# Performance work log

Hardware: AMD Instinct MI355X
Metric: run time of the kernel (lower is better)

## Reference

```python
import jax, jax.numpy as jnp
import numpy as np

D_STATE = 8
DT_RANK = 8  # ceil(128/16)


def _grouped_1x1(x, w):
    # x: (B,H,W,Cin), w: (g, Cout//g, Cin//g)
    B, H, W, _ = x.shape
    g, o, i = w.shape
    xg = x.reshape(B, H, W, g, i)
    return jnp.einsum('bhwgi,goi->bhwgo', xg, w).reshape(B, H, W, g * o)


def setup_inputs() -> dict:
    key = jax.random.key(0)
    ks = jax.random.split(key, 16)
    B, H, W, C = 8, 64, 64, 128
    g = 4
    D = 128  # expand_dim = d_inner
    N = D_STATE
    R = DT_RANK
    inp = {}
    inp['x'] = jax.random.normal(ks[0], (B, H, W, C), dtype=jnp.float32)
    inp['w1'] = jax.random.normal(ks[1], (g, D // g, C // g), dtype=jnp.float32) * 0.1
    inp['dw'] = jax.random.normal(ks[2], (3, 3, 1, D), dtype=jnp.float32) * 0.1  # HWIO depthwise
    inp['in_proj_w'] = jax.random.normal(ks[3], (2 * D, D), dtype=jnp.float32) * 0.05
    inp['conv1d_w'] = jax.random.normal(ks[4], (D, 3), dtype=jnp.float32) * 0.1
    inp['conv1d_b'] = jax.random.normal(ks[5], (D,), dtype=jnp.float32) * 0.05
    inp['x_proj_w'] = jax.random.normal(ks[6], (R + 2 * N, D), dtype=jnp.float32) * 0.05
    inp['dt_proj_w'] = jax.random.normal(ks[7], (D, R), dtype=jnp.float32) * 0.05
    inp['dt_proj_b'] = jax.random.normal(ks[8], (D,), dtype=jnp.float32) * 0.05
    inp['A_log'] = jnp.log(jnp.tile(jnp.arange(1, N + 1, dtype=jnp.float32)[None, :], (D, 1)))
    inp['D_param'] = jnp.ones((D,), dtype=jnp.float32)
    inp['out_proj_w'] = jax.random.normal(ks[9], (D, D), dtype=jnp.float32) * 0.05
    inp['gamma'] = jnp.ones((D,), dtype=jnp.float32)
    inp['beta'] = jnp.zeros((D,), dtype=jnp.float32)
    inp['w2'] = jax.random.normal(ks[10], (g, D // g, C // g), dtype=jnp.float32) * 0.1
    inp['wout'] = jax.random.normal(ks[11], (g, C // g, D // g), dtype=jnp.float32) * 0.1
    return inp


def _mamba(x_seq, in_proj_w, conv1d_w, conv1d_b, x_proj_w, dt_proj_w, dt_proj_b, A_log, D_param, out_proj_w):
    # x_seq: (B, L, D)
    B, L, D = x_seq.shape
    N, R = D_STATE, DT_RANK
    xz = jnp.einsum('bld,ed->ble', x_seq, in_proj_w)  # (B,L,2D)
    u, z = xz[..., :D], xz[..., D:]
    # causal depthwise conv1d, kernel=3, left pad 2 (torch: padding=2, slice [:L])
    up = jnp.pad(u, ((0, 0), (2, 0), (0, 0)))
    u = (up[:, 0:L] * conv1d_w[:, 0] + up[:, 1:L + 1] * conv1d_w[:, 1]
         + up[:, 2:L + 2] * conv1d_w[:, 2] + conv1d_b)
    u = jax.nn.silu(u)
    x_dbl = jnp.einsum('bld,ed->ble', u, x_proj_w)  # (B,L,R+2N)
    dt = x_dbl[..., :R]
    Bm = x_dbl[..., R:R + N]
    Cm = x_dbl[..., R + N:]
    delta = jax.nn.softplus(jnp.einsum('blr,dr->bld', dt, dt_proj_w) + dt_proj_b)  # (B,L,D)
    A = -jnp.exp(A_log)  # (D,N)

    def step(h, inp):
        d_t, u_t, b_t, c_t = inp  # (B,D),(B,D),(B,N),(B,N)
        dA = jnp.exp(d_t[..., None] * A)            # (B,D,N)
        h = dA * h + (d_t * u_t)[..., None] * b_t[:, None, :]
        y_t = jnp.einsum('bdn,bn->bd', h, c_t)
        return h, y_t

    h0 = jnp.zeros((B, D, N), dtype=x_seq.dtype)
    xs = (jnp.swapaxes(delta, 0, 1), jnp.swapaxes(u, 0, 1),
          jnp.swapaxes(Bm, 0, 1), jnp.swapaxes(Cm, 0, 1))
    _, ys = jax.lax.scan(step, h0, xs)              # ys: (L,B,D)
    y = jnp.swapaxes(ys, 0, 1) + u * D_param
    y = y * jax.nn.silu(z)
    return jnp.einsum('bld,ed->ble', y, out_proj_w)


def reference(x, w1, dw, in_proj_w, conv1d_w, conv1d_b, x_proj_w, dt_proj_w, dt_proj_b,
              A_log, D_param, out_proj_w, gamma, beta, w2, wout):
    B, H, W, C = x.shape
    D = dw.shape[-1]
    x1 = _grouped_1x1(x, w1)  # (B,H,W,D)
    x1 = jax.lax.conv_general_dilated(
        x1, dw, window_strides=(1, 1), padding='SAME',
        feature_group_count=D, dimension_numbers=('NHWC', 'HWIO', 'NHWC'))
    x1 = jax.nn.silu(x1)
    x1_seq = x1.reshape(B, H * W, D)
    x1_seq = _mamba(x1_seq, in_proj_w, conv1d_w, conv1d_b, x_proj_w,
                    dt_proj_w, dt_proj_b, A_log, D_param, out_proj_w)
    x1 = x1_seq.reshape(B, H, W, D)
    mu = jnp.mean(x1, axis=-1, keepdims=True)
    var = jnp.mean(jnp.square(x1 - mu), axis=-1, keepdims=True)
    x1 = (x1 - mu) * jax.lax.rsqrt(var + 1e-5) * gamma + beta
    x2 = jax.nn.silu(_grouped_1x1(x, w2))
    x_fuse = x1 * x2
    return _grouped_1x1(x_fuse, wout)  # (B,H,W,C)
```

## Files before the change

kernel.cpp:

```cpp
#include <hip/hip_runtime.h>
#include <math.h>

#define B_    8
#define C_    128
#define D_    128
#define L_    4096
#define NPOS_ 32768
#define NC_   128
#define S_    32
#define NB_   4194304
#define MFL_  1048576

typedef __attribute__((ext_vector_type(8))) short short8;
typedef __attribute__((ext_vector_type(4))) float f32x4;

__device__ __forceinline__ float siluf(float x) { return x / (1.f + __expf(-x)); }
__device__ __forceinline__ float softplusf(float x) {
    if (x > 20.f) return x;
    return log1pf(__expf(x));
}
__device__ __forceinline__ unsigned short f2bf(float f) {
    unsigned int u = __float_as_uint(f);
    u = (u + 0x7FFFu + ((u >> 16) & 1u)) >> 16;
    return (unsigned short)u;
}
__device__ __forceinline__ float bf2f(unsigned short h) {
    return __uint_as_float(((unsigned int)h) << 16);
}

__global__ __launch_bounds__(256) void k0_cvt(const float* __restrict__ inW,
                                              const float* __restrict__ OW,
                                              const float* __restrict__ xpw,
                                              unsigned short* __restrict__ inWb,
                                              unsigned short* __restrict__ OWb,
                                              unsigned short* __restrict__ xpwb) {
    for (int i = blockIdx.x * 256 + threadIdx.x; i < 52224; i += gridDim.x * 256) {
        if (i < 32768)      inWb[i] = f2bf(inW[i]);
        else if (i < 49152) OWb[i - 32768] = f2bf(OW[i - 32768]);
        else                xpwb[i - 49152] = f2bf(xpw[i - 49152]);
    }
}

__global__ __launch_bounds__(256) void k1_g1x1(const float* __restrict__ x,
                                               const float* __restrict__ w1,
                                               const float* __restrict__ w2,
                                               float* __restrict__ t1,
                                               float* __restrict__ x2s) {
    __shared__ float xs[16 * 128];
    int t = threadIdx.x;
    int d = t & 127, ph = t >> 7;
    int g = d >> 5, o = d & 31;
    float w1r[32], w2r[32];
    #pragma unroll
    for (int i = 0; i < 32; ++i) {
        w1r[i] = w1[g * 1024 + o * 32 + i];
        w2r[i] = w2[g * 1024 + o * 32 + i];
    }
    int pos0 = blockIdx.x * 64;
    for (int it = 0; it < 4; ++it) {
        int p0 = pos0 + it * 16;
        #pragma unroll
        for (int q = 0; q < 2; ++q) {
            int fi = t * 2 + q;
            *(float4*)&xs[fi * 4] = *(const float4*)&x[p0 * 128 + fi * 4];
        }
        __syncthreads();
        #pragma unroll
        for (int q = 0; q < 8; ++q) {
            int pl = ph * 8 + q;
            float a1 = 0.f, a2 = 0.f;
            const float* xr = &xs[pl * 128 + g * 32];
            #pragma unroll
            for (int i4 = 0; i4 < 8; ++i4) {
                float4 xv = *(const float4*)&xr[i4 * 4];
                a1 += xv.x * w1r[i4*4] + xv.y * w1r[i4*4+1] + xv.z * w1r[i4*4+2] + xv.w * w1r[i4*4+3];
                a2 += xv.x * w2r[i4*4] + xv.y * w2r[i4*4+1] + xv.z * w2r[i4*4+2] + xv.w * w2r[i4*4+3];
            }
            int pos = p0 + pl;
            t1[pos * 128 + d]  = a1;
            x2s[pos * 128 + d] = siluf(a2);
        }
        __syncthreads();
    }
}

__global__ __launch_bounds__(128) void k2_dwconv(const float* __restrict__ t1,
                                                 const float* __restrict__ dw,
                                                 unsigned short* __restrict__ x1cb) {
    int d = threadIdx.x;
    float dwr[9];
    #pragma unroll
    for (int k = 0; k < 9; ++k) dwr[k] = dw[k * 128 + d];
    int bid = blockIdx.x;
    int wt = bid & 7, ht = (bid >> 3) & 7, b = bid >> 6;
    int h0 = ht * 8, w0 = wt * 8;
    float rows[10][10];
    #pragma unroll
    for (int r = 0; r < 10; ++r) {
        int hh = h0 - 1 + r;
        bool hv = (hh >= 0) && (hh < 64);
        #pragma unroll
        for (int c = 0; c < 10; ++c) {
            int w = w0 - 1 + c;
            bool wvv = (w >= 0) && (w < 64);
            rows[r][c] = (hv && wvv) ? t1[((b * 64 + hh) * 64 + w) * 128 + d] : 0.f;
        }
    }
    #pragma unroll
    for (int hi = 0; hi < 8; ++hi) {
        #pragma unroll
        for (int wi = 0; wi < 8; ++wi) {
            float acc = rows[hi][wi]     * dwr[0] + rows[hi][wi+1]   * dwr[1] + rows[hi][wi+2]   * dwr[2]
                      + rows[hi+1][wi]   * dwr[3] + rows[hi+1][wi+1] * dwr[4] + rows[hi+1][wi+2] * dwr[5]
                      + rows[hi+2][wi]   * dwr[6] + rows[hi+2][wi+1] * dwr[7] + rows[hi+2][wi+2] * dwr[8];
            x1cb[((b * 64 + h0 + hi) * 64 + w0 + wi) * 128 + d] = f2bf(siluf(acc));
        }
    }
}

__global__ __launch_bounds__(256) void k3_mfma(const unsigned short* __restrict__ Abf,
                                               const unsigned short* __restrict__ Bbf,
                                               float* __restrict__ uraw,
                                               unsigned short* __restrict__ zb) {
    __shared__ unsigned short Al[128 * 72];
    __shared__ unsigned short Bl[128 * 72];
    int t = threadIdx.x;
    int mtile = blockIdx.x >> 1, ntile = blockIdx.x & 1;
    int pos0 = mtile * 128, n0g = ntile * 128;
    int lane = t & 63, wv = t >> 6;
    int m0 = (wv & 1) * 64, n0w = (wv >> 1) * 64;
    int lanem = lane & 15, laneq = lane >> 4;
    f32x4 acc[4][4];
    #pragma unroll
    for (int i = 0; i < 4; ++i)
        #pragma unroll
        for (int j = 0; j < 4; ++j) acc[i][j] = (f32x4){0.f, 0.f, 0.f, 0.f};
    for (int kc = 0; kc < 2; ++kc) {
        #pragma unroll
        for (int q = 0; q < 4; ++q) {
            int c = t + q * 256;
            int row = c >> 3, col = c & 7;
            *(int4*)&Al[row * 72 + col * 8] = *(const int4*)&Abf[(pos0 + row) * 128 + kc * 64 + col * 8];
            *(int4*)&Bl[row * 72 + col * 8] = *(const int4*)&Bbf[(n0g + row) * 128 + kc * 64 + col * 8];
        }
        __syncthreads();
        #pragma unroll
        for (int ks = 0; ks < 2; ++ks) {
            short8 af[4], bfr[4];
            #pragma unroll
            for (int mi = 0; mi < 4; ++mi)
                af[mi] = *(const short8*)&Al[(m0 + mi * 16 + lanem) * 72 + ks * 32 + laneq * 8];
            #pragma unroll
            for (int ni = 0; ni < 4; ++ni)
                bfr[ni] = *(const short8*)&Bl[(n0w + ni * 16 + lanem) * 72 + ks * 32 + laneq * 8];
            #pragma unroll
            for (int mi = 0; mi < 4; ++mi)
                #pragma unroll
                for (int ni = 0; ni < 4; ++ni)
                    acc[mi][ni] = __builtin_amdgcn_mfma_f32_16x16x32_bf16(af[mi], bfr[ni], acc[mi][ni], 0, 0, 0);
        }
        __syncthreads();
    }
    #pragma unroll
    for (int mi = 0; mi < 4; ++mi)
        #pragma unroll
        for (int ni = 0; ni < 4; ++ni)
            #pragma unroll
            for (int r = 0; r < 4; ++r) {
                int m = pos0 + m0 + mi * 16 + laneq * 4 + r;
                int n = n0w + ni * 16 + lanem;
                if (ntile) zb[m * 128 + n] = f2bf(acc[mi][ni][r]);
                else       uraw[m * 128 + n] = acc[mi][ni][r];
            }
}

__global__ __launch_bounds__(256) void k4_convproj(const float* __restrict__ uraw,
                                                   const float* __restrict__ cw,
                                                   const float* __restrict__ cb,
                                                   const unsigned short* __restrict__ xpwb,
                                                   const float* __restrict__ dtw,
                                                   const float* __restrict__ dtb,
                                                   float* __restrict__ u,
                                                   float* __restrict__ delta,
                                                   float* __restrict__ Bm,
                                                   float* __restrict__ Cm) {
    __shared__ unsigned short uA[64 * 136];
    __shared__ unsigned short xB[32 * 136];
    __shared__ float xdb[64 * 36];
    int t = threadIdx.x;
    int d = t & 127, ph = t >> 7;
    for (int i = t; i < 32 * 128; i += 256) {
        int n = i >> 7, k = i & 127;
        xB[n * 136 + k] = (n < 24) ? xpwb[n * 128 + k] : (unsigned short)0;
    }
    float cw0 = cw[d * 3 + 0], cw1 = cw[d * 3 + 1], cw2 = cw[d * 3 + 2], cbr = cb[d];
    float dtwr[8];
    #pragma unroll
    for (int r = 0; r < 8; ++r) dtwr[r] = dtw[d * 8 + r];
    float dtbr = dtb[d];

    int gpos0 = blockIdx.x * 64;
    int ll0 = (gpos0 & 4095) + ph * 32;
    int base = (gpos0 + ph * 32) * 128 + d;
    float ur0 = (ll0 >= 2) ? uraw[base - 256] : 0.f;
    float ur1 = (ll0 >= 1) ? uraw[base - 128] : 0.f;
    #pragma unroll
    for (int q = 0; q < 32; ++q) {
        float urq = uraw[base + q * 128];
        float us = siluf(ur0 * cw0 + ur1 * cw1 + urq * cw2 + cbr);
        u[base + q * 128] = us;
        uA[(ph * 32 + q) * 136 + d] = f2bf(us);
        ur0 = ur1; ur1 = urq;
    }
    __syncthreads();
    int lane = t & 63, wv = t >> 6;
    int lanem = lane & 15, laneq = lane >> 4;
    f32x4 accx[2];
    accx[0] = (f32x4){0.f, 0.f, 0.f, 0.f};
    accx[1] = (f32x4){0.f, 0.f, 0.f, 0.f};
    #pragma unroll
    for (int ks = 0; ks < 4; ++ks) {
        short8 af = *(const short8*)&uA[(wv * 16 + lanem) * 136 + ks * 32 + laneq * 8];
        #pragma unroll
        for (int nj = 0; nj < 2; ++nj) {
            short8 bfr = *(const short8*)&xB[(nj * 16 + lanem) * 136 + ks * 32 + laneq * 8];
            accx[nj] = __builtin_amdgcn_mfma_f32_16x16x32_bf16(af, bfr, accx[nj], 0, 0, 0);
        }
    }
    #pragma unroll
    for (int nj = 0; nj < 2; ++nj)
        #pragma unroll
        for (int r = 0; r < 4; ++r)
            xdb[(wv * 16 + laneq * 4 + r) * 36 + nj * 16 + lanem] = accx[nj][r];
    __syncthreads();
    #pragma unroll
    for (int q = 0; q < 32; ++q) {
        int pl = ph * 32 + q;
        float dt = dtbr;
        #pragma unroll
        for (int r = 0; r < 8; ++r) dt += xdb[pl * 36 + r] * dtwr[r];
        delta[base + q * 128] = softplusf(dt);
    }
    for (int i = t; i < 1024; i += 256) {
        int p = i >> 4, j = i & 15;
        float v = xdb[p * 36 + 8 + j];
        int gp = gpos0 + p;
        if (j < 8) Bm[gp * 8 + j] = v;
        else       Cm[gp * 8 + (j - 8)] = v;
    }
}

__global__ __launch_bounds__(128) void k5_scan1(const float* __restrict__ delta,
                                                const float* __restrict__ u,
                                                const float* __restrict__ Bm,
                                                const float* __restrict__ A_log,
                                                float* __restrict__ cA,
                                                float* __restrict__ cB) {
    int d = threadIdx.x;
    int bc = blockIdx.x;
    int b = bc >> 7, c = bc & 127;
    float Ar[8];
    #pragma unroll
    for (int n = 0; n < 8; ++n) Ar[n] = -__expf(A_log[d * 8 + n]);
    float h[8], ap[8];
    #pragma unroll
    for (int n = 0; n < 8; ++n) { h[n] = 0.f; ap[n] = 1.f; }
    int base  = (b * L_ + c * S_) * 128 + d;
    int bbase = (b * L_ + c * S_) * 8;
    for (int s = 0; s < S_; ++s) {
        float dl = delta[base + s * 128];
        float uv = u[base + s * 128];
        float du = dl * uv;
        float4 bm0 = *(const float4*)&Bm[bbase + s * 8];
        float4 bm1 = *(const float4*)&Bm[bbase + s * 8 + 4];
        float a;
        a = __expf(dl * Ar[0]); ap[0] *= a; h[0] = a * h[0] + du * bm0.x;
        a = __expf(dl * Ar[1]); ap[1] *= a; h[1] = a * h[1] + du * bm0.y;
        a = __expf(dl * Ar[2]); ap[2] *= a; h[2] = a * h[2] + du * bm0.z;
        a = __expf(dl * Ar[3]); ap[3] *= a; h[3] = a * h[3] + du * bm0.w;
        a = __expf(dl * Ar[4]); ap[4] *= a; h[4] = a * h[4] + du * bm1.x;
        a = __expf(dl * Ar[5]); ap[5] *= a; h[5] = a * h[5] + du * bm1.y;
        a = __expf(dl * Ar[6]); ap[6] *= a; h[6] = a * h[6] + du * bm1.z;
        a = __expf(dl * Ar[7]); ap[7] *= a; h[7] = a * h[7] + du * bm1.w;
    }
    int obase = (bc * 128 + d) * 8;
    *(float4*)&cA[obase]     = make_float4(ap[0], ap[1], ap[2], ap[3]);
    *(float4*)&cA[obase + 4] = make_float4(ap[4], ap[5], ap[6], ap[7]);
    *(float4*)&cB[obase]     = make_float4(h[0], h[1], h[2], h[3]);
    *(float4*)&cB[obase + 4] = make_float4(h[4], h[5], h[6], h[7]);
}

__global__ __launch_bounds__(128) void k6_scan2(const float* __restrict__ cA,
                                                const float* __restrict__ cB,
                                                float* __restrict__ carry) {
    int b = blockIdx.x >> 3;
    int slice = blockIdx.x & 7;
    int dn = slice * 128 + threadIdx.x;
    float h = 0.f;
    for (int c = 0; c < NC_; ++c) {
        int idx = (b * NC_ + c) * 1024 + dn;
        float a  = cA[idx];
        float bv = cB[idx];
        carry[idx] = h;
        h = a * h + bv;
    }
}

__global__ __launch_bounds__(128) void k7_scan3(const float* __restrict__ delta,
                                                const float* __restrict__ u,
                                                const float* __restrict__ Bm,
                                                const float* __restrict__ Cm,
                                                const unsigned short* __restrict__ zb,
                                                const float* __restrict__ A_log,
                                                const float* __restrict__ Dp,
                                                const float* __restrict__ carry,
                                                unsigned short* __restrict__ ybf) {
    int d = threadIdx.x;
    int bc = blockIdx.x;
    int b = bc >> 7, c = bc & 127;
    float Ar[8];
    #pragma unroll
    for (int n = 0; n < 8; ++n) Ar[n] = -__expf(A_log[d * 8 + n]);
    float Dpr = Dp[d];
    int cbase = (bc * 128 + d) * 8;
    float4 h0 = *(const float4*)&carry[cbase];
    float4 h1 = *(const float4*)&carry[cbase + 4];
    float h[8] = {h0.x, h0.y, h0.z, h0.w, h1.x, h1.y, h1.z, h1.w};
    int base  = (b * L_ + c * S_) * 128 + d;
    int bbase = (b * L_ + c * S_) * 8;
    for (int s = 0; s < S_; ++s) {
        float dl = delta[base + s * 128];
        float uv = u[base + s * 128];
        float zv = bf2f(zb[base + s * 128]);
        float du = dl * uv;
        float4 bm0 = *(const float4*)&Bm[bbase + s * 8];
        float4 bm1 = *(const float4*)&Bm[bbase + s * 8 + 4];
        float4 cm0 = *(const float4*)&Cm[bbase + s * 8];
        float4 cm1 = *(const float4*)&Cm[bbase + s * 8 + 4];
        float a;
        a = __expf(dl * Ar[0]); h[0] = a * h[0] + du * bm0.x;
        a = __expf(dl * Ar[1]); h[1] = a * h[1] + du * bm0.y;
        a = __expf(dl * Ar[2]); h[2] = a * h[2] + du * bm0.z;
        a = __expf(dl * Ar[3]); h[3] = a * h[3] + du * bm0.w;
        a = __expf(dl * Ar[4]); h[4] = a * h[4] + du * bm1.x;
        a = __expf(dl * Ar[5]); h[5] = a * h[5] + du * bm1.y;
        a = __expf(dl * Ar[6]); h[6] = a * h[6] + du * bm1.z;
        a = __expf(dl * Ar[7]); h[7] = a * h[7] + du * bm1.w;
        float yv = h[0] * cm0.x + h[1] * cm0.y + h[2] * cm0.z + h[3] * cm0.w
                 + h[4] * cm1.x + h[5] * cm1.y + h[6] * cm1.z + h[7] * cm1.w;
        yv = (yv + uv * Dpr) * siluf(zv);
        ybf[base + s * 128] = f2bf(yv);
    }
}

__global__ __launch_bounds__(256) void k8a_mfma(const unsigned short* __restrict__ Abf,
                                                const unsigned short* __restrict__ Bbf,
                                                float* __restrict__ xz) {
    __shared__ unsigned short Al[128 * 72];
    __shared__ unsigned short Bl[128 * 72];
    int t = threadIdx.x;
    int pos0 = blockIdx.x * 128;
    int lane = t & 63, wv = t >> 6;
    int m0 = (wv & 1) * 64, n0w = (wv >> 1) * 64;
    int lanem = lane & 15, laneq = lane >> 4;
    f32x4 acc[4][4];
    #pragma unroll
    for (int i = 0; i < 4; ++i)
        #pragma unroll
        for (int j = 0; j < 4; ++j) acc[i][j] = (f32x4){0.f, 0.f, 0.f, 0.f};
    for (int kc = 0; kc < 2; ++kc) {
        #pragma unroll
        for (int q = 0; q < 4; ++q) {
            int c = t + q * 256;
            int row = c >> 3, col = c & 7;
            *(int4*)&Al[row * 72 + col * 8] = *(const int4*)&Abf[(pos0 + row) * 128 + kc * 64 + col * 8];
            *(int4*)&Bl[row * 72 + col * 8] = *(const int4*)&Bbf[row * 128 + kc * 64 + col * 8];
        }
        __syncthreads();
        #pragma unroll
        for (int ks = 0; ks < 2; ++ks) {
            short8 af[4], bfr[4];
            #pragma unroll
            for (int mi = 0; mi < 4; ++mi)
                af[mi] = *(const short8*)&Al[(m0 + mi * 16 + lanem) * 72 + ks * 32 + laneq * 8];
            #pragma unroll
            for (int ni = 0; ni < 4; ++ni)
                bfr[ni] = *(const short8*)&Bl[(n0w + ni * 16 + lanem) * 72 + ks * 32 + laneq * 8];
            #pragma unroll
            for (int mi = 0; mi < 4; ++mi)
                #pragma unroll
                for (int ni = 0; ni < 4; ++ni)
                    acc[mi][ni] = __builtin_amdgcn_mfma_f32_16x16x32_bf16(af[mi], bfr[ni], acc[mi][ni], 0, 0, 0);
        }
        __syncthreads();
    }
    #pragma unroll
    for (int mi = 0; mi < 4; ++mi)
        #pragma unroll
        for (int ni = 0; ni < 4; ++ni)
            #pragma unroll
            for (int r = 0; r < 4; ++r) {
                int m = pos0 + m0 + mi * 16 + laneq * 4 + r;
                int n = n0w + ni * 16 + lanem;
                xz[m * 128 + n] = acc[mi][ni][r];
            }
}

__global__ __launch_bounds__(256) void k8b_epi(const float* __restrict__ xz,
                                               const float* __restrict__ gamma,
                                               const float* __restrict__ beta,
                                               const float* __restrict__ x2s,
                                               const float* __restrict__ wout,
                                               float* __restrict__ out) {
    __shared__ float wt[32 * 128];
    __shared__ float xfs[32 * 132];
    int t  = threadIdx.x;
    int te = t & 31, tp = t >> 5;
    for (int idx = t; idx < 4096; idx += 256) {
        int i = idx >> 7, c = idx & 127;
        wt[idx] = wout[(c >> 5) * 1024 + (c & 31) * 32 + i];
    }
    float gr[4], br[4];
    #pragma unroll
    for (int j = 0; j < 4; ++j) { gr[j] = gamma[te + 32 * j]; br[j] = beta[te + 32 * j]; }

    int pos0 = blockIdx.x * 32;
    float acc[4][4];
    #pragma unroll
    for (int i = 0; i < 4; ++i) {
        int pos = pos0 + tp * 4 + i;
        #pragma unroll
        for (int j = 0; j < 4; ++j) acc[i][j] = xz[pos * 128 + te + 32 * j];
    }
    #pragma unroll
    for (int i = 0; i < 4; ++i) {
        float s  = acc[i][0] + acc[i][1] + acc[i][2] + acc[i][3];
        float s2 = acc[i][0]*acc[i][0] + acc[i][1]*acc[i][1] + acc[i][2]*acc[i][2] + acc[i][3]*acc[i][3];
        #pragma unroll
        for (int off = 16; off >= 1; off >>= 1) {
            s  += __shfl_xor(s, off, 64);
            s2 += __shfl_xor(s2, off, 64);
        }
        float m = s * (1.f / 128.f);
        float var = s2 * (1.f / 128.f) - m * m;
        float rstd = rsqrtf(var + 1e-5f);
        int pos = pos0 + tp * 4 + i;
        #pragma unroll
        for (int j = 0; j < 4; ++j) {
            int e = te + 32 * j;
            float v = (acc[i][j] - m) * rstd * gr[j] + br[j];
            v *= x2s[pos * 128 + e];
            xfs[(tp * 4 + i) * 132 + e] = v;
        }
    }
    __syncthreads();
    #pragma unroll
    for (int i = 0; i < 4; ++i) {
        int pos = pos0 + tp * 4 + i;
        const float* xr = &xfs[(tp * 4 + i) * 132];
        float a2[4] = {0.f, 0.f, 0.f, 0.f};
        for (int ii = 0; ii < 32; ++ii) {
            #pragma unroll
            for (int j = 0; j < 4; ++j)
                a2[j] += xr[j * 32 + ii] * wt[ii * 128 + 32 * j + te];
        }
        #pragma unroll
        for (int j = 0; j < 4; ++j) out[pos * 128 + 32 * j + te] = a2[j];
    }
}

extern "C" void kernel_launch(void* const* d_in, const int* in_sizes, int n_in,
                              void* d_out, int out_size, void* d_ws, size_t ws_size,
                              hipStream_t stream) {
    (void)in_sizes; (void)n_in; (void)out_size; (void)ws_size;
    const float* x         = (const float*)d_in[0];
    const float* w1        = (const float*)d_in[1];
    const float* dw        = (const float*)d_in[2];
    const float* in_proj_w = (const float*)d_in[3];
    const float* conv1d_w  = (const float*)d_in[4];
    const float* conv1d_b  = (const float*)d_in[5];
    const float* x_proj_w  = (const float*)d_in[6];
    const float* dt_proj_w = (const float*)d_in[7];
    const float* dt_proj_b = (const float*)d_in[8];
    const float* A_log     = (const float*)d_in[9];
    const float* D_param   = (const float*)d_in[10];
    const float* out_proj_w= (const float*)d_in[11];
    const float* gamma     = (const float*)d_in[12];
    const float* beta      = (const float*)d_in[13];
    const float* w2        = (const float*)d_in[14];
    const float* wout      = (const float*)d_in[15];
    float* out = (float*)d_out;

    float* ws = (float*)d_ws;
    float* t1    = ws;
    float* x2s   = ws + 4 * (size_t)MFL_;
    float* uraw  = ws + 8 * (size_t)MFL_;
    unsigned short* zb = (unsigned short*)(ws + 12 * (size_t)MFL_);
    float* delta = ws + 16 * (size_t)MFL_;
    unsigned short* x1cb = (unsigned short*)(ws + 16 * (size_t)MFL_);
    unsigned short* ybf  = (unsigned short*)(ws + 20 * (size_t)MFL_);
    float* Bm    = ws + 22 * (size_t)MFL_;
    float* Cm    = Bm + (size_t)NPOS_ * 8;
    float* cA    = Cm + (size_t)NPOS_ * 8;
    float* cB    = cA + (size_t)MFL_;
    float* carry = cB + (size_t)MFL_;
    unsigned short* inWb = (unsigned short*)(carry + (size_t)MFL_);
    unsigned short* OWb  = inWb + 32768;
    unsigned short* xpwb = OWb + 16384;
    float* u  = t1;
    float* xz = uraw;

    k0_cvt<<<64, 256, 0, stream>>>(in_proj_w, out_proj_w, x_proj_w, inWb, OWb, xpwb);
    k1_g1x1<<<512, 256, 0, stream>>>(x, w1, w2, t1, x2s);
    k2_dwconv<<<512, 128, 0, stream>>>(t1, dw, x1cb);
    k3_mfma<<<512, 256, 0, stream>>>(x1cb, inWb, uraw, zb);
    k4_convproj<<<512, 256, 0, stream>>>(uraw, conv1d_w, conv1d_b, xpwb,
                                         dt_proj_w, dt_proj_b, u, delta, Bm, Cm);
    k5_scan1<<<1024, 128, 0, stream>>>(delta, u, Bm, A_log, cA, cB);
    k6_scan2<<<64, 128, 0, stream>>>(cA, cB, carry);
    k7_scan3<<<1024, 128, 0, stream>>>(delta, u, Bm, Cm, zb, A_log, D_param, carry, ybf);
    k8a_mfma<<<256, 256, 0, stream>>>(ybf, OWb, xz);
    k8b_epi<<<1024, 256, 0, stream>>>(xz, gamma, beta, x2s, wout, out);
}
```

Baseline: 250.9 us.

## Fuse scan phase-1 into conv/proj kernel, fuse out-proj with LayerNorm epilogue, bf16 intermediates

Stores the t1 and uraw intermediates as bf16 instead of fp32, which halves their memory traffic. The chunk-local scan (old k5) moves into the conv/x_proj kernel so delta, u and B are used from registers and shared memory, and u is no longer written. k7 recomputes u from urawb using the causal conv. The out_proj MFMA GEMM is fused with the LayerNorm, gating and grouped output projection through shared memory, which removes the fp32 xz round trip. The cost is extra bf16 rounding error, the recompute of u, and more shared memory per block.

```diff
diff --git a/kernel.cpp b/kernel.cpp
--- a/kernel.cpp
+++ b/kernel.cpp
@@ -8,7 +8,6 @@
 #define NPOS_ 32768
 #define NC_   128
 #define S_    32
-#define NB_   4194304
 #define MFL_  1048576
 
 typedef __attribute__((ext_vector_type(8))) short short8;
@@ -44,7 +43,7 @@
 __global__ __launch_bounds__(256) void k1_g1x1(const float* __restrict__ x,
                                                const float* __restrict__ w1,
                                                const float* __restrict__ w2,
-                                               float* __restrict__ t1,
+                                               unsigned short* __restrict__ t1b,
                                                float* __restrict__ x2s) {
     __shared__ float xs[16 * 128];
     int t = threadIdx.x;
@@ -77,14 +76,14 @@
                 a2 += xv.x * w2r[i4*4] + xv.y * w2r[i4*4+1] + xv.z * w2r[i4*4+2] + xv.w * w2r[i4*4+3];
             }
             int pos = p0 + pl;
-            t1[pos * 128 + d]  = a1;
+            t1b[pos * 128 + d] = f2bf(a1);
             x2s[pos * 128 + d] = siluf(a2);
         }
         __syncthreads();
     }
 }
 
-__global__ __launch_bounds__(128) void k2_dwconv(const float* __restrict__ t1,
+__global__ __launch_bounds__(128) void k2_dwconv(const unsigned short* __restrict__ t1b,
                                                  const float* __restrict__ dw,
                                                  unsigned short* __restrict__ x1cb) {
     int d = threadIdx.x;
@@ -103,7 +102,7 @@
         for (int c = 0; c < 10; ++c) {
             int w = w0 - 1 + c;
             bool wvv = (w >= 0) && (w < 64);
-            rows[r][c] = (hv && wvv) ? t1[((b * 64 + hh) * 64 + w) * 128 + d] : 0.f;
+            rows[r][c] = (hv && wvv) ? bf2f(t1b[((b * 64 + hh) * 64 + w) * 128 + d]) : 0.f;
         }
     }
     #pragma unroll
@@ -120,7 +119,7 @@
 
 __global__ __launch_bounds__(256) void k3_mfma(const unsigned short* __restrict__ Abf,
                                                const unsigned short* __restrict__ Bbf,
-                                               float* __restrict__ uraw,
+                                               unsigned short* __restrict__ urawb,
                                                unsigned short* __restrict__ zb) {
     __shared__ unsigned short Al[128 * 72];
     __shared__ unsigned short Bl[128 * 72];
@@ -161,6 +160,7 @@
         }
         __syncthreads();
     }
+    unsigned short* dst = ntile ? zb : urawb;
     #pragma unroll
     for (int mi = 0; mi < 4; ++mi)
         #pragma unroll
@@ -169,21 +169,22 @@
             for (int r = 0; r < 4; ++r) {
                 int m = pos0 + m0 + mi * 16 + laneq * 4 + r;
                 int n = n0w + ni * 16 + lanem;
-                if (ntile) zb[m * 128 + n] = f2bf(acc[mi][ni][r]);
-                else       uraw[m * 128 + n] = acc[mi][ni][r];
+                dst[m * 128 + n] = f2bf(acc[mi][ni][r]);
             }
 }
 
-__global__ __launch_bounds__(256) void k4_convproj(const float* __restrict__ uraw,
-                                                   const float* __restrict__ cw,
-                                                   const float* __restrict__ cb,
-                                                   const unsigned short* __restrict__ xpwb,
-                                                   const float* __restrict__ dtw,
-                                                   const float* __restrict__ dtb,
-                                                   float* __restrict__ u,
-                                                   float* __restrict__ delta,
-                                                   float* __restrict__ Bm,
-                                                   float* __restrict__ Cm) {
+__global__ __launch_bounds__(256) void k45_convscan(const unsigned short* __restrict__ urawb,
+                                                    const float* __restrict__ cw,
+                                                    const float* __restrict__ cb,
+                                                    const unsigned short* __restrict__ xpwb,
+                                                    const float* __restrict__ dtw,
+                                                    const float* __restrict__ dtb,
+                                                    const float* __restrict__ A_log,
+                                                    float* __restrict__ delta,
+                                                    float* __restrict__ Bm,
+                                                    float* __restrict__ Cm,
+                                                    float* __restrict__ cA,
+                                                    float* __restrict__ cB) {
     __shared__ unsigned short uA[64 * 136];
     __shared__ unsigned short xB[32 * 136];
     __shared__ float xdb[64 * 36];
@@ -198,18 +199,22 @@
     #pragma unroll
     for (int r = 0; r < 8; ++r) dtwr[r] = dtw[d * 8 + r];
     float dtbr = dtb[d];
+    float Ar[8];
+    #pragma unroll
+    for (int n = 0; n < 8; ++n) Ar[n] = -__expf(A_log[d * 8 + n]);
 
     int gpos0 = blockIdx.x * 64;
     int ll0 = (gpos0 & 4095) + ph * 32;
     int base = (gpos0 + ph * 32) * 128 + d;
-    float ur0 = (ll0 >= 2) ? uraw[base - 256] : 0.f;
-    float ur1 = (ll0 >= 1) ? uraw[base - 128] : 0.f;
+    float ur0 = (ll0 >= 2) ? bf2f(urawb[base - 256]) : 0.f;
+    float ur1 = (ll0 >= 1) ? bf2f(urawb[base - 128]) : 0.f;
+    float us[32];
     #pragma unroll
     for (int q = 0; q < 32; ++q) {
-        float urq = uraw[base + q * 128];
-        float us = siluf(ur0 * cw0 + ur1 * cw1 + urq * cw2 + cbr);
-        u[base + q * 128] = us;
-        uA[(ph * 32 + q) * 136 + d] = f2bf(us);
+        float urq = bf2f(urawb[base + q * 128]);
+        float v = siluf(ur0 * cw0 + ur1 * cw1 + urq * cw2 + cbr);
+        us[q] = v;
+        uA[(ph * 32 + q) * 136 + d] = f2bf(v);
         ur0 = ur1; ur1 = urq;
     }
     __syncthreads();
@@ -233,14 +238,32 @@
         for (int r = 0; r < 4; ++r)
             xdb[(wv * 16 + laneq * 4 + r) * 36 + nj * 16 + lanem] = accx[nj][r];
     __syncthreads();
+    float h[8], ap[8];
+    #pragma unroll
+    for (int n = 0; n < 8; ++n) { h[n] = 0.f; ap[n] = 1.f; }
     #pragma unroll
     for (int q = 0; q < 32; ++q) {
         int pl = ph * 32 + q;
         float dt = dtbr;
         #pragma unroll
         for (int r = 0; r < 8; ++r) dt += xdb[pl * 36 + r] * dtwr[r];
-        delta[base + q * 128] = softplusf(dt);
-    }
+        float dl = softplusf(dt);
+        delta[base + q * 128] = dl;
+        float du = dl * us[q];
+        #pragma unroll
+        for (int n = 0; n < 8; ++n) {
+            float a = __expf(dl * Ar[n]);
+            ap[n] *= a;
+            h[n] = a * h[n] + du * xdb[pl * 36 + 8 + n];
+        }
+    }
+    int bH = gpos0 >> 12;
+    int c  = ((gpos0 & 4095) >> 5) + ph;
+    int obase = ((bH * 128 + c) * 128 + d) * 8;
+    *(float4*)&cA[obase]     = make_float4(ap[0], ap[1], ap[2], ap[3]);
+    *(float4*)&cA[obase + 4] = make_float4(ap[4], ap[5], ap[6], ap[7]);
+    *(float4*)&cB[obase]     = make_float4(h[0], h[1], h[2], h[3]);
+    *(float4*)&cB[obase + 4] = make_float4(h[4], h[5], h[6], h[7]);
     for (int i = t; i < 1024; i += 256) {
         int p = i >> 4, j = i & 15;
         float v = xdb[p * 36 + 8 + j];
@@ -248,46 +271,6 @@
         if (j < 8) Bm[gp * 8 + j] = v;
         else       Cm[gp * 8 + (j - 8)] = v;
     }
-}
-
-__global__ __launch_bounds__(128) void k5_scan1(const float* __restrict__ delta,
-                                                const float* __restrict__ u,
-                                                const float* __restrict__ Bm,
-                                                const float* __restrict__ A_log,
-                                                float* __restrict__ cA,
-                                                float* __restrict__ cB) {
-    int d = threadIdx.x;
-    int bc = blockIdx.x;
-    int b = bc >> 7, c = bc & 127;
-    float Ar[8];
-    #pragma unroll
-    for (int n = 0; n < 8; ++n) Ar[n] = -__expf(A_log[d * 8 + n]);
-    float h[8], ap[8];
-    #pragma unroll
-    for (int n = 0; n < 8; ++n) { h[n] = 0.f; ap[n] = 1.f; }
-    int base  = (b * L_ + c * S_) * 128 + d;
-    int bbase = (b * L_ + c * S_) * 8;
-    for (int s = 0; s < S_; ++s) {
-        float dl = delta[base + s * 128];
-        float uv = u[base + s * 128];
-        float du = dl * uv;
-        float4 bm0 = *(const float4*)&Bm[bbase + s * 8];
-        float4 bm1 = *(const float4*)&Bm[bbase + s * 8 + 4];
-        float a;
-        a = __expf(dl * Ar[0]); ap[0] *= a; h[0] = a * h[0] + du * bm0.x;
-        a = __expf(dl * Ar[1]); ap[1] *= a; h[1] = a * h[1] + du * bm0.y;
-        a = __expf(dl * Ar[2]); ap[2] *= a; h[2] = a * h[2] + du * bm0.z;
-        a = __expf(dl * Ar[3]); ap[3] *= a; h[3] = a * h[3] + du * bm0.w;
-        a = __expf(dl * Ar[4]); ap[4] *= a; h[4] = a * h[4] + du * bm1.x;
-        a = __expf(dl * Ar[5]); ap[5] *= a; h[5] = a * h[5] + du * bm1.y;
-        a = __expf(dl * Ar[6]); ap[6] *= a; h[6] = a * h[6] + du * bm1.z;
-        a = __expf(dl * Ar[7]); ap[7] *= a; h[7] = a * h[7] + du * bm1.w;
-    }
-    int obase = (bc * 128 + d) * 8;
-    *(float4*)&cA[obase]     = make_float4(ap[0], ap[1], ap[2], ap[3]);
-    *(float4*)&cA[obase + 4] = make_float4(ap[4], ap[5], ap[6], ap[7]);
-    *(float4*)&cB[obase]     = make_float4(h[0], h[1], h[2], h[3]);
-    *(float4*)&cB[obase + 4] = make_float4(h[4], h[5], h[6], h[7]);
 }
 
 __global__ __launch_bounds__(128) void k6_scan2(const float* __restrict__ cA,
@@ -307,7 +290,9 @@
 }
 
 __global__ __launch_bounds__(128) void k7_scan3(const float* __restrict__ delta,
-                                                const float* __restrict__ u,
+                                                const unsigned short* __restrict__ urawb,
+                                                const float* __restrict__ cw,
+                                                const float* __restrict__ cb,
                                                 const float* __restrict__ Bm,
                                                 const float* __restrict__ Cm,
                                                 const unsigned short* __restrict__ zb,
@@ -322,15 +307,21 @@
     #pragma unroll
     for (int n = 0; n < 8; ++n) Ar[n] = -__expf(A_log[d * 8 + n]);
     float Dpr = Dp[d];
+    float cw0 = cw[d * 3 + 0], cw1 = cw[d * 3 + 1], cw2 = cw[d * 3 + 2], cbr = cb[d];
     int cbase = (bc * 128 + d) * 8;
     float4 h0 = *(const float4*)&carry[cbase];
     float4 h1 = *(const float4*)&carry[cbase + 4];
     float h[8] = {h0.x, h0.y, h0.z, h0.w, h1.x, h1.y, h1.z, h1.w};
-    int base  = (b * L_ + c * S_) * 128 + d;
-    int bbase = (b * L_ + c * S_) * 8;
+    int l0 = c * S_;
+    int base  = (b * L_ + l0) * 128 + d;
+    int bbase = (b * L_ + l0) * 8;
+    float ur0 = (l0 >= 2) ? bf2f(urawb[base - 256]) : 0.f;
+    float ur1 = (l0 >= 1) ? bf2f(urawb[base - 128]) : 0.f;
     for (int s = 0; s < S_; ++s) {
+        float urq = bf2f(urawb[base + s * 128]);
+        float uv = siluf(ur0 * cw0 + ur1 * cw1 + urq * cw2 + cbr);
+        ur0 = ur1; ur1 = urq;
         float dl = delta[base + s * 128];
-        float uv = u[base + s * 128];
         float zv = bf2f(zb[base + s * 128]);
         float du = dl * uv;
         float4 bm0 = *(const float4*)&Bm[bbase + s * 8];
@@ -353,89 +344,71 @@
     }
 }
 
-__global__ __launch_bounds__(256) void k8a_mfma(const unsigned short* __restrict__ Abf,
-                                                const unsigned short* __restrict__ Bbf,
-                                                float* __restrict__ xz) {
-    __shared__ unsigned short Al[128 * 72];
+__global__ __launch_bounds__(256) void k89_outfuse(const unsigned short* __restrict__ ybf,
+                                                   const unsigned short* __restrict__ OWb,
+                                                   const float* __restrict__ gamma,
+                                                   const float* __restrict__ beta,
+                                                   const float* __restrict__ x2s,
+                                                   const float* __restrict__ wout,
+                                                   float* __restrict__ out) {
+    __shared__ unsigned short Al[64 * 72];
     __shared__ unsigned short Bl[128 * 72];
+    __shared__ float xzl[64 * 132];
+    __shared__ float wt2[128 * 36];
     int t = threadIdx.x;
-    int pos0 = blockIdx.x * 128;
+    int pos0 = blockIdx.x * 64;
+    for (int i = t; i < 4096; i += 256) {
+        int cc = i >> 5, ii = i & 31;
+        wt2[cc * 36 + ii] = wout[i];
+    }
     int lane = t & 63, wv = t >> 6;
-    int m0 = (wv & 1) * 64, n0w = (wv >> 1) * 64;
     int lanem = lane & 15, laneq = lane >> 4;
-    f32x4 acc[4][4];
-    #pragma unroll
-    for (int i = 0; i < 4; ++i)
-        #pragma unroll
-        for (int j = 0; j < 4; ++j) acc[i][j] = (f32x4){0.f, 0.f, 0.f, 0.f};
+    f32x4 acc[8];
+    #pragma unroll
+    for (int i = 0; i < 8; ++i) acc[i] = (f32x4){0.f, 0.f, 0.f, 0.f};
     for (int kc = 0; kc < 2; ++kc) {
         #pragma unroll
+        for (int q = 0; q < 2; ++q) {
+            int ccc = t + q * 256;
+            int row = ccc >> 3, col = ccc & 7;
+            *(int4*)&Al[row * 72 + col * 8] = *(const int4*)&ybf[(pos0 + row) * 128 + kc * 64 + col * 8];
+        }
+        #pragma unroll
         for (int q = 0; q < 4; ++q) {
-            int c = t + q * 256;
-            int row = c >> 3, col = c & 7;
-            *(int4*)&Al[row * 72 + col * 8] = *(const int4*)&Abf[(pos0 + row) * 128 + kc * 64 + col * 8];
-            *(int4*)&Bl[row * 72 + col * 8] = *(const int4*)&Bbf[row * 128 + kc * 64 + col * 8];
+            int ccc = t + q * 256;
+            int row = ccc >> 3, col = ccc & 7;
+            *(int4*)&Bl[row * 72 + col * 8] = *(const int4*)&OWb[row * 128 + kc * 64 + col * 8];
         }
         __syncthreads();
         #pragma unroll
         for (int ks = 0; ks < 2; ++ks) {
-            short8 af[4], bfr[4];
-            #pragma unroll
-            for (int mi = 0; mi < 4; ++mi)
-                af[mi] = *(const short8*)&Al[(m0 + mi * 16 + lanem) * 72 + ks * 32 + laneq * 8];
-            #pragma unroll
-            for (int ni = 0; ni < 4; ++ni)
-                bfr[ni] = *(const short8*)&Bl[(n0w + ni * 16 + lanem) * 72 + ks * 32 + laneq * 8];
-            #pragma unroll
-            for (int mi = 0; mi < 4; ++mi)
-                #pragma unroll
-                for (int ni = 0; ni < 4; ++ni)
-                    acc[mi][ni] = __builtin_amdgcn_mfma_f32_16x16x32_bf16(af[mi], bfr[ni], acc[mi][ni], 0, 0, 0);
-        }
-        __syncthreads();
-    }
-    #pragma unroll
-    for (int mi = 0; mi < 4; ++mi)
-        #pragma unroll
-        for (int ni = 0; ni < 4; ++ni)
-            #pragma unroll
-            for (int r = 0; r < 4; ++r) {
-                int m = pos0 + m0 + mi * 16 + laneq * 4 + r;
-                int n = n0w + ni * 16 + lanem;
-                xz[m * 128 + n] = acc[mi][ni][r];
+            short8 af = *(const short8*)&Al[(wv * 16 + lanem) * 72 + ks * 32 + laneq * 8];
+            #pragma unroll
+            for (int ni = 0; ni < 8; ++ni) {
+                short8 bfr = *(const short8*)&Bl[(ni * 16 + lanem) * 72 + ks * 32 + laneq * 8];
+                acc[ni] = __builtin_amdgcn_mfma_f32_16x16x32_bf16(af, bfr, acc[ni], 0, 0, 0);
             }
-}
-
-__global__ __launch_bounds__(256) void k8b_epi(const float* __restrict__ xz,
-                                               const float* __restrict__ gamma,
-                                               const float* __restrict__ beta,
-                                               const float* __restrict__ x2s,
-                                               const float* __restrict__ wout,
-                                               float* __restrict__ out) {
-    __shared__ float wt[32 * 128];
-    __shared__ float xfs[32 * 132];
-    int t  = threadIdx.x;
+        }
+        __syncthreads();
+    }
+    #pragma unroll
+    for (int ni = 0; ni < 8; ++ni)
+        #pragma unroll
+        for (int r = 0; r < 4; ++r)
+            xzl[(wv * 16 + laneq * 4 + r) * 132 + ni * 16 + lanem] = acc[ni][r];
+    __syncthreads();
     int te = t & 31, tp = t >> 5;
-    for (int idx = t; idx < 4096; idx += 256) {
-        int i = idx >> 7, c = idx & 127;
-        wt[idx] = wout[(c >> 5) * 1024 + (c & 31) * 32 + i];
-    }
     float gr[4], br[4];
     #pragma unroll
     for (int j = 0; j < 4; ++j) { gr[j] = gamma[te + 32 * j]; br[j] = beta[te + 32 * j]; }
-
-    int pos0 = blockIdx.x * 32;
-    float acc[4][4];
-    #pragma unroll
-    for (int i = 0; i < 4; ++i) {
-        int pos = pos0 + tp * 4 + i;
-        #pragma unroll
-        for (int j = 0; j < 4; ++j) acc[i][j] = xz[pos * 128 + te + 32 * j];
-    }
-    #pragma unroll
-    for (int i = 0; i < 4; ++i) {
-        float s  = acc[i][0] + acc[i][1] + acc[i][2] + acc[i][3];
-        float s2 = acc[i][0]*acc[i][0] + acc[i][1]*acc[i][1] + acc[i][2]*acc[i][2] + acc[i][3]*acc[i][3];
+    #pragma unroll
+    for (int i = 0; i < 8; ++i) {
+        int row = tp * 8 + i;
+        float v[4];
+        #pragma unroll
+        for (int j = 0; j < 4; ++j) v[j] = xzl[row * 132 + te + 32 * j];
+        float s  = v[0] + v[1] + v[2] + v[3];
+        float s2 = v[0]*v[0] + v[1]*v[1] + v[2]*v[2] + v[3]*v[3];
         #pragma unroll
         for (int off = 16; off >= 1; off >>= 1) {
             s  += __shfl_xor(s, off, 64);
@@ -444,25 +417,29 @@
         float m = s * (1.f / 128.f);
         float var = s2 * (1.f / 128.f) - m * m;
         float rstd = rsqrtf(var + 1e-5f);
-        int pos = pos0 + tp * 4 + i;
+        int pos = pos0 + row;
         #pragma unroll
         for (int j = 0; j < 4; ++j) {
-            int e = te + 32 * j;
-            float v = (acc[i][j] - m) * rstd * gr[j] + br[j];
-            v *= x2s[pos * 128 + e];
-            xfs[(tp * 4 + i) * 132 + e] = v;
+            float vv = (v[j] - m) * rstd * gr[j] + br[j];
+            vv *= x2s[pos * 128 + te + 32 * j];
+            xzl[row * 132 + te + 32 * j] = vv;
         }
     }
     __syncthreads();
     #pragma unroll
-    for (int i = 0; i < 4; ++i) {
-        int pos = pos0 + tp * 4 + i;
-        const float* xr = &xfs[(tp * 4 + i) * 132];
+    for (int i = 0; i < 8; ++i) {
+        int row = tp * 8 + i;
+        int pos = pos0 + row;
+        const float* xr = &xzl[row * 132];
         float a2[4] = {0.f, 0.f, 0.f, 0.f};
-        for (int ii = 0; ii < 32; ++ii) {
-            #pragma unroll
-            for (int j = 0; j < 4; ++j)
-                a2[j] += xr[j * 32 + ii] * wt[ii * 128 + 32 * j + te];
+        #pragma unroll
+        for (int i4 = 0; i4 < 8; ++i4) {
+            #pragma unroll
+            for (int j = 0; j < 4; ++j) {
+                float4 xv = *(const float4*)&xr[j * 32 + i4 * 4];
+                float4 wv4 = *(const float4*)&wt2[(j * 32 + te) * 36 + i4 * 4];
+                a2[j] += xv.x * wv4.x + xv.y * wv4.y + xv.z * wv4.z + xv.w * wv4.w;
+            }
         }
         #pragma unroll
         for (int j = 0; j < 4; ++j) out[pos * 128 + 32 * j + te] = a2[j];
@@ -492,14 +469,14 @@
     float* out = (float*)d_out;
 
     float* ws = (float*)d_ws;
-    float* t1    = ws;
-    float* x2s   = ws + 4 * (size_t)MFL_;
-    float* uraw  = ws + 8 * (size_t)MFL_;
-    unsigned short* zb = (unsigned short*)(ws + 12 * (size_t)MFL_);
-    float* delta = ws + 16 * (size_t)MFL_;
-    unsigned short* x1cb = (unsigned short*)(ws + 16 * (size_t)MFL_);
-    unsigned short* ybf  = (unsigned short*)(ws + 20 * (size_t)MFL_);
-    float* Bm    = ws + 22 * (size_t)MFL_;
+    float* x2s   = ws;
+    float* delta = ws + 4 * (size_t)MFL_;
+    unsigned short* t1b   = (unsigned short*)(ws + 8  * (size_t)MFL_);
+    unsigned short* x1cb  = (unsigned short*)(ws + 10 * (size_t)MFL_);
+    unsigned short* urawb = (unsigned short*)(ws + 12 * (size_t)MFL_);
+    unsigned short* zb    = (unsigned short*)(ws + 14 * (size_t)MFL_);
+    unsigned short* ybf   = (unsigned short*)(ws + 16 * (size_t)MFL_);
+    float* Bm    = ws + 18 * (size_t)MFL_;
     float* Cm    = Bm + (size_t)NPOS_ * 8;
     float* cA    = Cm + (size_t)NPOS_ * 8;
     float* cB    = cA + (size_t)MFL_;
@@ -507,18 +484,16 @@
     unsigned short* inWb = (unsigned short*)(carry + (size_t)MFL_);
     unsigned short* OWb  = inWb + 32768;
     unsigned short* xpwb = OWb + 16384;
-    float* u  = t1;
-    float* xz = uraw;
 
     k0_cvt<<<64, 256, 0, stream>>>(in_proj_w, out_proj_w, x_proj_w, inWb, OWb, xpwb);
-    k1_g1x1<<<512, 256, 0, stream>>>(x, w1, w2, t1, x2s);
-    k2_dwconv<<<512, 128, 0, stream>>>(t1, dw, x1cb);
-    k3_mfma<<<512, 256, 0, stream>>>(x1cb, inWb, uraw, zb);
-    k4_convproj<<<512, 256, 0, stream>>>(uraw, conv1d_w, conv1d_b, xpwb,
-                                         dt_proj_w, dt_proj_b, u, delta, Bm, Cm);
-    k5_scan1<<<1024, 128, 0, stream>>>(delta, u, Bm, A_log, cA, cB);
+    k1_g1x1<<<512, 256, 0, stream>>>(x, w1, w2, t1b, x2s);
+    k2_dwconv<<<512, 128, 0, stream>>>(t1b, dw, x1cb);
+    k3_mfma<<<512, 256, 0, stream>>>(x1cb, inWb, urawb, zb);
+    k45_convscan<<<512, 256, 0, stream>>>(urawb, conv1d_w, conv1d_b, xpwb,
+                                          dt_proj_w, dt_proj_b, A_log,
+                                          delta, Bm, Cm, cA, cB);
     k6_scan2<<<64, 128, 0, stream>>>(cA, cB, carry);
-    k7_scan3<<<1024, 128, 0, stream>>>(delta, u, Bm, Cm, zb, A_log, D_param, carry, ybf);
-    k8a_mfma<<<256, 256, 0, stream>>>(ybf, OWb, xz);
-    k8b_epi<<<1024, 256, 0, stream>>>(xz, gamma, beta, x2s, wout, out);
-}
+    k7_scan3<<<1024, 128, 0, stream>>>(delta, urawb, conv1d_w, conv1d_b,
+                                       Bm, Cm, zb, A_log, D_param, carry, ybf);
+    k89_outfuse<<<512, 256, 0, stream>>>(ybf, OWb, gamma, beta, x2s, wout, out);
+}
```

After: 285.8 us. 13.9% more time.
